# Kernel optimization log

Measured on AMD Instinct MI355X. Metric: run time of the kernel, lower is better.

Reference implementation:

```python
import jax, jax.numpy as jnp
import numpy as np


def _lin_interp(x, out_size):
    # x: [..., T_in]; matches torch F.interpolate(mode='linear', align_corners=False)
    t_in = x.shape[-1]
    scale = t_in / out_size
    pos = (jnp.arange(out_size, dtype=jnp.float32) + 0.5) * scale - 0.5
    pos = jnp.clip(pos, 0.0, t_in - 1)
    lo = jnp.floor(pos).astype(jnp.int32)
    hi = jnp.minimum(lo + 1, t_in - 1)
    w = (pos - lo.astype(jnp.float32)).astype(x.dtype)
    return x[..., lo] * (1.0 - w) + x[..., hi] * w


def _lin_init(k, fan_in, shape):
    lim = 1.0 / np.sqrt(fan_in)
    return jax.random.uniform(k, shape, jnp.float32, -lim, lim)


def setup_inputs() -> dict:
    key = jax.random.key(0)
    ks = jax.random.split(key, 32)
    B, T, NMEL = 8, 1024, 80
    TV, H, W = 32, 112, 112
    S = 4  # max_speakers
    d = {}
    d['audio_input'] = jax.random.normal(ks[0], (B, T, NMEL), jnp.float32)
    d['video_input'] = jax.random.normal(ks[1], (B, TV, 3, H, W), jnp.float32)
    d['w_ae'] = _lin_init(ks[2], 80, (80, 256)); d['b_ae'] = _lin_init(ks[3], 80, (256,))
    d['ln_g'] = jnp.ones((256,), jnp.float32); d['ln_b'] = jnp.zeros((256,), jnp.float32)
    d['w_a1'] = _lin_init(ks[4], 256, (256, 512)); d['b_a1'] = _lin_init(ks[5], 256, (512,))
    d['w_a2'] = _lin_init(ks[6], 512, (512, 256)); d['b_a2'] = _lin_init(ks[7], 512, (256,))
    fan = 3 * 7 * 7
    d['conv_w'] = _lin_init(ks[8], fan, (64, 3, 7, 7)); d['conv_b'] = _lin_init(ks[9], fan, (64,))
    d['w_vfc'] = _lin_init(ks[10], 64, (64, 256)); d['b_vfc'] = _lin_init(ks[11], 64, (256,))
    d['w_f1'] = _lin_init(ks[12], 512, (512, 512)); d['b_f1'] = _lin_init(ks[13], 512, (512,))
    d['w_f2'] = _lin_init(ks[14], 512, (512, 256)); d['b_f2'] = _lin_init(ks[15], 512, (256,))
    d['heads_w'] = _lin_init(ks[16], 256, (S, 256, 80)); d['heads_b'] = _lin_init(ks[17], 256, (S, 80))
    d['w_spk'] = _lin_init(ks[18], 256, (256, S)); d['b_spk'] = _lin_init(ks[19], 256, (S,))
    return d


def reference(audio_input, video_input, w_ae, b_ae, ln_g, ln_b, w_a1, b_a1, w_a2, b_a2,
              conv_w, conv_b, w_vfc, b_vfc, w_f1, b_f1, w_f2, b_f2,
              heads_w, heads_b, w_spk, b_spk):
    # ---- audio branch ----
    a = audio_input @ w_ae + b_ae                      # [B,T,256]
    mu = a.mean(-1, keepdims=True)
    var = a.var(-1, keepdims=True)
    a = (a - mu) * jax.lax.rsqrt(var + 1e-5) * ln_g + ln_b
    a = jax.nn.relu(a @ w_a1 + b_a1) @ w_a2 + b_a2     # dropout is identity at eval
    # ---- video branch ----
    B, TV, C, H, W = video_input.shape
    v = video_input.reshape(B * TV, C, H, W)
    v = jax.lax.conv_general_dilated(v, conv_w, (2, 2), [(3, 3), (3, 3)],
                                     dimension_numbers=('NCHW', 'OIHW', 'NCHW'))
    v = v + conv_b[None, :, None, None]
    v = v.mean((2, 3))                                  # AdaptiveAvgPool2d((1,1))
    v = (v @ w_vfc + b_vfc).reshape(B, TV, 256)
    T = a.shape[1]
    if TV != T:
        v = _lin_interp(v.transpose(0, 2, 1), T).transpose(0, 2, 1)  # [B,T,256]
    # ---- fusion ----
    f = jnp.concatenate([a, v], axis=-1)                # [B,T,512]
    f = jax.nn.relu(f @ w_f1 + b_f1) @ w_f2 + b_f2      # [B,T,256]
    # ---- per-speaker heads as one batched GEMM ----
    specs = jnp.einsum('btd,sdo->bsto', f, heads_w) + heads_b[None, :, None, :]  # [B,S,T,80]
    # ---- specs -> waveforms (vectorized over batch x speakers) ----
    S = specs.shape[1]
    wave_len = T * 160  # samples_per_frame = 160
    noise = jax.random.normal(jax.random.key(1234), (B, S, wave_len), jnp.float32) * 0.1
    energy = _lin_interp(specs.sum(-1), wave_len)       # [B,S,wave_len]
    waveforms = noise * (energy * 0.5 + 0.5)
    # ---- speaker classifier ----
    speaker_logits = f.mean(1) @ w_spk + b_spk          # [B,S]
    return waveforms, specs, speaker_logits
```

## Files before the change

kernel.cpp:

```cpp
#include <hip/hip_runtime.h>
#include <hip/hip_bf16.h>
#include <math.h>

typedef _Float16 f16;
typedef f16 f16x8 __attribute__((ext_vector_type(8)));
typedef f16 f16x4 __attribute__((ext_vector_type(4)));
typedef float f32x4 __attribute__((ext_vector_type(4)));

template<int MT, int RELU, int OUT, int XTRA = 0>
__global__ __launch_bounds__(256) void hgemm(
    const f16* __restrict__ A, const f16* __restrict__ Wt,
    const float* __restrict__ bias,
    void* __restrict__ Cout, int ldc, int col_off,
    int N, int K, float* __restrict__ colsum)
{
  static_assert(MT == 64 || MT == 128, "MT");
  constexpr int MI = MT / 32;
  if (XTRA) {
    if (blockIdx.y == 4) {
      const float* v256 = colsum;
      f16* fb = (f16*)Cout;
      const int base = blockIdx.x * 16384 + (int)threadIdx.x;
#pragma unroll 4
      for (int i = 0; i < 64; i++) {
        const int idx = base + i * 256;
        const int c = idx & 255;
        const int t = (idx >> 8) & 1023;
        const int b = idx >> 18;
        float pos = ((float)t + 0.5f) * 0.03125f - 0.5f;
        pos = fminf(fmaxf(pos, 0.0f), 31.0f);
        const int lo = (int)floorf(pos);
        int hi = lo + 1; if (hi > 31) hi = 31;
        const float w = pos - (float)lo;
        const float vl = v256[(size_t)(b * 32 + lo) * 256 + c];
        const float vh = v256[(size_t)(b * 32 + hi) * 256 + c];
        fb[(size_t)(b * 1024 + t) * 512 + 256 + c] = (f16)(vl * (1.0f - w) + vh * w);
      }
      return;
    }
  }
  __shared__ __align__(16) f16 As[2][MT * 64];
  __shared__ __align__(16) f16 Bs[2][64 * 64];
  const int tid = threadIdx.x;
  const int wave = tid >> 6, lane = tid & 63;
  const int wm = (wave >> 1) * (MT / 2);
  const int wn = (wave & 1) * 32;
  const int m0 = blockIdx.x * MT;
  const int n0 = blockIdx.y * 64;
  const int q = lane >> 4, r16 = lane & 15;

  const int rA0 = tid >> 3, gA0 = tid & 7;
  const f16* pA = A + (size_t)(m0 + rA0) * K + gA0 * 8;
  const f16* pB = Wt + (size_t)(n0 + rA0) * K + gA0 * 8;
  const int sbase = rA0 * 128 + ((gA0 ^ (rA0 & 7)) * 16);

  f32x4 acc[MI][2];
#pragma unroll
  for (int mi = 0; mi < MI; mi++)
#pragma unroll
    for (int ni = 0; ni < 2; ni++) acc[mi][ni] = (f32x4)0.f;

  f16x8 ar[MI], br[2];
#pragma unroll
  for (int j = 0; j < MI; j++) ar[j] = *(const f16x8*)(pA + (size_t)j * 32 * K);
#pragma unroll
  for (int j = 0; j < 2; j++) br[j] = *(const f16x8*)(pB + (size_t)j * 32 * K);

  const int iters = K >> 6;
  int p = 0;
  for (int it = 0; it < iters; it++) {
#pragma unroll
    for (int j = 0; j < MI; j++)
      *(f16x8*)((char*)As[p] + sbase + j * 4096) = ar[j];
#pragma unroll
    for (int j = 0; j < 2; j++)
      *(f16x8*)((char*)Bs[p] + sbase + j * 4096) = br[j];
    if (it + 1 < iters) {
      const int ko = (it + 1) << 6;
#pragma unroll
      for (int j = 0; j < MI; j++) ar[j] = *(const f16x8*)(pA + (size_t)j * 32 * K + ko);
#pragma unroll
      for (int j = 0; j < 2; j++) br[j] = *(const f16x8*)(pB + (size_t)j * 32 * K + ko);
    }
    __syncthreads();
#pragma unroll
    for (int h = 0; h < 2; h++) {
      const int kg = h * 4 + q;
      f16x8 af[MI], bf[2];
#pragma unroll
      for (int mi = 0; mi < MI; mi++) {
        const int row = wm + mi * 16 + r16;
        af[mi] = *(const f16x8*)((char*)As[p] + row * 128 + ((kg ^ (row & 7)) * 16));
      }
#pragma unroll
      for (int ni = 0; ni < 2; ni++) {
        const int row = wn + ni * 16 + r16;
        bf[ni] = *(const f16x8*)((char*)Bs[p] + row * 128 + ((kg ^ (row & 7)) * 16));
      }
#pragma unroll
      for (int mi = 0; mi < MI; mi++)
#pragma unroll
        for (int ni = 0; ni < 2; ni++)
          acc[mi][ni] = __builtin_amdgcn_mfma_f32_16x16x32_f16(
              af[mi], bf[ni], acc[mi][ni], 0, 0, 0);
    }
    p ^= 1;
  }

#pragma unroll
  for (int ni = 0; ni < 2; ni++) {
    const int n = n0 + wn + ni * 16 + r16;
    const float bv = bias[n];
    float csum = 0.f;
#pragma unroll
    for (int mi = 0; mi < MI; mi++) {
#pragma unroll
      for (int rr = 0; rr < 4; rr++) {
        const int m = m0 + wm + mi * 16 + q * 4 + rr;
        float v = acc[mi][ni][rr] + bv;
        if (RELU) v = fmaxf(v, 0.f);
        if (OUT == 2) csum += v;
        ((f16*)Cout)[(size_t)m * ldc + col_off + n] = (f16)v;
      }
    }
    if (OUT == 2) {
      csum += __shfl_xor(csum, 16);
      csum += __shfl_xor(csum, 32);
      if (q == 0) atomicAdd(&colsum[(m0 >> 10) * 256 + n], csum);
    }
  }
}

__global__ __launch_bounds__(256) void prep_video_kernel(
    const float* __restrict__ video, float* __restrict__ Sg,
    const float* __restrict__ w_ae, const float* __restrict__ w_a1,
    const float* __restrict__ w_a2, const float* __restrict__ w_f1,
    const float* __restrict__ w_f2, const float* __restrict__ heads_w,
    const float* __restrict__ heads_b,
    f16* __restrict__ wae_t, f16* __restrict__ wa1_t,
    f16* __restrict__ wa2_t, f16* __restrict__ wf1_t, f16* __restrict__ wf2_t,
    f16* __restrict__ wh_t, float* __restrict__ bp, float* __restrict__ colsum)
{
  if (blockIdx.x < 768) {
    const int img = blockIdx.x;
    const float* p = video + (size_t)img * 12544;
    __shared__ __align__(16) float imgc[28 * 112];
    __shared__ float rowS[2][112];
    __shared__ float c0s[112], c1s[112], c109s[112], c110s[112], c111s[112];
    __shared__ float base[14];
    __shared__ float sE[7], sO[7];
    const int t = threadIdx.x;
#pragma unroll 1
    for (int c = 0; c < 4; c++) {
      for (int i = t; i < 784; i += 256)
        ((float4*)imgc)[i] = ((const float4*)(p + c * 3136))[i];
      __syncthreads();
      if (t < 56) {
        const int rl = t >> 1;
        const int r = c * 28 + rl;
        const int par = t & 1;
        const float* rp = imgc + rl * 112 + par;
        float s = 0.f;
#pragma unroll
        for (int i = 0; i < 56; i++) s += rp[2 * i];
        rowS[par][r] = s;
        if (par == 0) { c0s[r] = rp[0]; c110s[r] = rp[110]; }
        else { c1s[r] = rp[0]; c109s[r] = rp[108]; c111s[r] = rp[110]; }
      }
      __syncthreads();
    }
    if (t < 14) {
      const int arr = t >> 1;
      const int rp = t & 1;
      const float* src = (arr == 0) ? rowS[0] : (arr == 1) ? rowS[1] :
                         (arr == 2) ? c0s : (arr == 3) ? c1s :
                         (arr == 4) ? c109s : (arr == 5) ? c110s : c111s;
      float s = 0.f;
      for (int r = rp; r < 112; r += 2) s += src[r];
      base[t] = s;
    }
    __syncthreads();
    if (t < 7) {
      float se, so;
      switch (t) {
        case 0: se = base[2] - base[8] - base[12]; so = base[3] - base[9] - base[13]; break;
        case 1: se = base[0] - base[10];           so = base[1] - base[11];           break;
        case 2: se = base[2] - base[12];           so = base[3] - base[13];           break;
        case 3: se = base[0];                      so = base[1];                      break;
        case 4: se = base[2];                      so = base[3];                      break;
        case 5: se = base[0] - base[4];            so = base[1] - base[5];            break;
        default: se = base[2] - base[6];           so = base[3] - base[7];            break;
      }
      sE[t] = se; sO[t] = so;
    }
    __syncthreads();
    if (t < 49) {
      const int kh = t / 7, kw = t % 7;
      auto ccol = [&](int r) -> float {
        switch (kw) {
          case 0: return rowS[1][r] - c109s[r] - c111s[r];
          case 1: return rowS[0][r] - c110s[r];
          case 2: return rowS[1][r] - c111s[r];
          case 3: return rowS[0][r];
          case 4: return rowS[1][r];
          case 5: return rowS[0][r] - c0s[r];
          default: return rowS[1][r] - c1s[r];
        }
      };
      float v;
      switch (kh) {
        case 0: v = sO[kw] - ccol(109) - ccol(111); break;
        case 1: v = sE[kw] - ccol(110);             break;
        case 2: v = sO[kw] - ccol(111);             break;
        case 3: v = sE[kw];                         break;
        case 4: v = sO[kw];                         break;
        case 5: v = sE[kw] - ccol(0);               break;
        default: v = sO[kw] - ccol(1);              break;
      }
      Sg[(size_t)img * 49 + t] = v;
    }
    return;
  }
  int idx = (blockIdx.x - 768) * 256 + threadIdx.x;
  if (idx < 32768) {
    const int n = idx >> 7, k = idx & 127;
    wae_t[idx] = (f16)(k < 80 ? w_ae[k * 256 + n] : 0.f);
    return;
  }
  idx -= 32768;
  if (idx < 131072) { const int n = idx >> 8, k = idx & 255; wa1_t[idx] = (f16)w_a1[k * 512 + n]; return; }
  idx -= 131072;
  if (idx < 131072) { const int n = idx >> 9, k = idx & 511; wa2_t[idx] = (f16)w_a2[k * 256 + n]; return; }
  idx -= 131072;
  if (idx < 262144) { const int n = idx >> 9, k = idx & 511; wf1_t[idx] = (f16)w_f1[k * 512 + n]; return; }
  idx -= 262144;
  if (idx < 131072) { const int n = idx >> 9, k = idx & 511; wf2_t[idx] = (f16)w_f2[k * 256 + n]; return; }
  idx -= 131072;
  if (idx < 81920) {
    const int n = idx >> 8, d = idx & 255;
    const int s = n / 80, o = n - s * 80;
    wh_t[idx] = (f16)heads_w[(size_t)(s * 256 + d) * 80 + o];
    return;
  }
  idx -= 81920;
  if (idx < 320) { bp[idx] = heads_b[idx]; return; }
  idx -= 320;
  if (idx < 2048) colsum[idx] = 0.f;
}

__global__ __launch_bounds__(256) void vpool_aeln_kernel(
    const float* __restrict__ Sg, const float* __restrict__ conv_w,
    const float* __restrict__ conv_b, const float* __restrict__ w_vfc,
    const float* __restrict__ b_vfc, float* __restrict__ v256,
    const float* __restrict__ audio, const f16* __restrict__ wae_t,
    const float* __restrict__ b_ae, const float* __restrict__ ln_g,
    const float* __restrict__ ln_b, f16* __restrict__ a1)
{
  __shared__ __align__(16) f16 As[64 * 128];
  __shared__ __align__(16) f16 Bs[256 * 128];
  const int tid = threadIdx.x;
  if (blockIdx.x < 256) {
    float* vp = (float*)As;
    const int n = blockIdx.x;
    if (tid < 64) {
      float acc = 0.f;
      const float* s = Sg + (size_t)n * 147;
#pragma unroll 7
      for (int k = 0; k < 147; k++) acc = fmaf(conv_w[tid * 147 + k], s[k], acc);
      vp[tid] = conv_b[tid] + acc * (1.0f / 3136.0f);
    }
    __syncthreads();
    float acc = 0.f;
#pragma unroll
    for (int k = 0; k < 64; k++) acc = fmaf(vp[k], w_vfc[k * 256 + tid], acc);
    v256[(size_t)n * 256 + tid] = acc + b_vfc[tid];
    return;
  }
  const int m0 = (blockIdx.x - 256) * 64;
  const int wave = tid >> 6, lane = tid & 63;
  const int q = lane >> 4, r16 = lane & 15;
#pragma unroll
  for (int c = tid; c < 1024; c += 256) {
    const int row = c >> 4, g = c & 15;
    f16x8 val = (f16x8)(f16)0.f;
    if (g < 10) {
      const float* src = audio + (size_t)(m0 + row) * 80 + g * 8;
      const float4 u = *(const float4*)src;
      const float4 w = *(const float4*)(src + 4);
      val[0] = (f16)u.x; val[1] = (f16)u.y; val[2] = (f16)u.z; val[3] = (f16)u.w;
      val[4] = (f16)w.x; val[5] = (f16)w.y; val[6] = (f16)w.z; val[7] = (f16)w.w;
    }
    *(f16x8*)((char*)As + row * 256 + ((g ^ (row & 7)) * 16)) = val;
  }
#pragma unroll
  for (int c = tid; c < 4096; c += 256) {
    const int row = c >> 4, g = c & 15;
    *(f16x8*)((char*)Bs + row * 256 + ((g ^ (row & 7)) * 16)) =
        *(const f16x8*)(wae_t + (size_t)row * 128 + g * 8);
  }
  __syncthreads();
  const int wm = wave * 16;
  f32x4 acc[16];
#pragma unroll
  for (int nf = 0; nf < 16; nf++) acc[nf] = (f32x4)0.f;
#pragma unroll
  for (int kf = 0; kf < 4; kf++) {
    const int kg = kf * 4 + q;
    const int ar = wm + r16;
    const f16x8 af = *(const f16x8*)((char*)As + ar * 256 + ((kg ^ (ar & 7)) * 16));
#pragma unroll
    for (int nf = 0; nf < 16; nf++) {
      const int br = nf * 16 + r16;
      const f16x8 bf = *(const f16x8*)((char*)Bs + br * 256 + ((kg ^ (br & 7)) * 16));
      acc[nf] = __builtin_amdgcn_mfma_f32_16x16x32_f16(af, bf, acc[nf], 0, 0, 0);
    }
  }
  float rs[4] = {0.f, 0.f, 0.f, 0.f};
  float rq[4] = {0.f, 0.f, 0.f, 0.f};
#pragma unroll
  for (int nf = 0; nf < 16; nf++) {
    const float bv = b_ae[nf * 16 + r16];
#pragma unroll
    for (int rr = 0; rr < 4; rr++) {
      const float v = acc[nf][rr] + bv;
      acc[nf][rr] = v;
      rs[rr] += v; rq[rr] += v * v;
    }
  }
#pragma unroll
  for (int off = 1; off < 16; off <<= 1) {
#pragma unroll
    for (int rr = 0; rr < 4; rr++) {
      rs[rr] += __shfl_xor(rs[rr], off);
      rq[rr] += __shfl_xor(rq[rr], off);
    }
  }
  float mu[4], ri[4];
#pragma unroll
  for (int rr = 0; rr < 4; rr++) {
    mu[rr] = rs[rr] * (1.0f / 256.0f);
    const float var = rq[rr] * (1.0f / 256.0f) - mu[rr] * mu[rr];
    ri[rr] = rsqrtf(var + 1e-5f);
  }
#pragma unroll
  for (int nf = 0; nf < 16; nf++) {
    const int col = nf * 16 + r16;
    const float g = ln_g[col], b = ln_b[col];
#pragma unroll
    for (int rr = 0; rr < 4; rr++) {
      const int row = m0 + wm + q * 4 + rr;
      a1[(size_t)row * 256 + col] = (f16)((acc[nf][rr] - mu[rr]) * ri[rr] * g + b);
    }
  }
}

__global__ __launch_bounds__(256) void heads_energy_kernel(
    const f16* __restrict__ A, const f16* __restrict__ Wt,
    const float* __restrict__ bias, float* __restrict__ specs,
    float* __restrict__ energy)
{
  __shared__ __align__(16) f16 As[64 * 256];
  __shared__ __align__(16) f16 Bs[80 * 256];
  const int tid = threadIdx.x;
  const int s = blockIdx.y;
  const int m0 = blockIdx.x * 64;
  const int wave = tid >> 6, lane = tid & 63;
  const int q = lane >> 4, r16 = lane & 15;
#pragma unroll
  for (int c = tid; c < 2048; c += 256) {
    const int row = c >> 5, g = c & 31;
    *(f16x8*)((char*)As + row * 512 + ((g ^ (row & 7)) * 16)) =
        *(const f16x8*)(A + (size_t)(m0 + row) * 256 + g * 8);
  }
#pragma unroll
  for (int c = tid; c < 2560; c += 256) {
    const int row = c >> 5, g = c & 31;
    *(f16x8*)((char*)Bs + row * 512 + ((g ^ (row & 7)) * 16)) =
        *(const f16x8*)(Wt + (size_t)(s * 80 + row) * 256 + g * 8);
  }
  __syncthreads();
  const int wm = wave * 16;
  f32x4 acc[5];
#pragma unroll
  for (int nf = 0; nf < 5; nf++) acc[nf] = (f32x4)0.f;
#pragma unroll
  for (int kf = 0; kf < 8; kf++) {
    const int kg = kf * 4 + q;
    const int ar = wm + r16;
    const f16x8 af = *(const f16x8*)((char*)As + ar * 512 + ((kg ^ (ar & 7)) * 16));
#pragma unroll
    for (int nf = 0; nf < 5; nf++) {
      const int br = nf * 16 + r16;
      const f16x8 bf = *(const f16x8*)((char*)Bs + br * 512 + ((kg ^ (br & 7)) * 16));
      acc[nf] = __builtin_amdgcn_mfma_f32_16x16x32_f16(af, bf, acc[nf], 0, 0, 0);
    }
  }
  float bv[5];
#pragma unroll
  for (int nf = 0; nf < 5; nf++) bv[nf] = bias[s * 80 + nf * 16 + r16];
  float rs[4] = {0.f, 0.f, 0.f, 0.f};
#pragma unroll
  for (int rr = 0; rr < 4; rr++) {
    const int row = m0 + wm + q * 4 + rr;
    const int b_ = row >> 10, t_ = row & 1023;
    float* dst = specs + ((size_t)((b_ * 4 + s) * 1024 + t_)) * 80;
#pragma unroll
    for (int nf = 0; nf < 5; nf++) {
      const float v = acc[nf][rr] + bv[nf];
      rs[rr] += v;
      dst[nf * 16 + r16] = v;
    }
  }
#pragma unroll
  for (int off = 1; off < 16; off <<= 1) {
#pragma unroll
    for (int rr = 0; rr < 4; rr++) rs[rr] += __shfl_xor(rs[rr], off);
  }
  if (r16 == 0) {
#pragma unroll
    for (int rr = 0; rr < 4; rr++) {
      const int row = m0 + wm + q * 4 + rr;
      const int b_ = row >> 10, t_ = row & 1023;
      energy[((b_ * 4 + s) << 10) + t_] = rs[rr];
    }
  }
}

__device__ __forceinline__ unsigned rotl32(unsigned x, int d) {
  return (x << d) | (x >> (32 - d));
}

__device__ __forceinline__ float erfinv_fast(float x) {
  const float t = (1.0f - x) * (1.0f + x);
  float w = -__logf(t);
  float p;
  if (w < 5.0f) {
    w = w - 2.5f;
    p = 2.81022636e-08f;
    p = fmaf(p, w, 3.43273939e-07f);
    p = fmaf(p, w, -3.5233877e-06f);
    p = fmaf(p, w, -4.39150654e-06f);
    p = fmaf(p, w, 0.00021858087f);
    p = fmaf(p, w, -0.00125372503f);
    p = fmaf(p, w, -0.00417768164f);
    p = fmaf(p, w, 0.246640727f);
    p = fmaf(p, w, 1.50140941f);
  } else {
    w = sqrtf(w) - 3.0f;
    p = -0.000200214257f;
    p = fmaf(p, w, 0.000100950558f);
    p = fmaf(p, w, 0.00134934322f);
    p = fmaf(p, w, -0.00367342844f);
    p = fmaf(p, w, 0.00573950773f);
    p = fmaf(p, w, -0.0076224613f);
    p = fmaf(p, w, 0.00943887047f);
    p = fmaf(p, w, 1.00167406f);
    p = fmaf(p, w, 2.83297682f);
  }
  return p * x;
}

__global__ __launch_bounds__(256) void waveform_kernel(
    const float* __restrict__ energy, float* __restrict__ out,
    const float* __restrict__ colsum, const float* __restrict__ w_spk,
    const float* __restrict__ b_spk, float* __restrict__ logits)
{
  if (blockIdx.x == 5120) {
    const int idx = threadIdx.x;
    if (idx < 32) {
      const int b = idx >> 2, s = idx & 3;
      const float* cs = colsum + b * 256;
      float acc = 0.f;
#pragma unroll 8
      for (int d = 0; d < 256; d++)
        acc = fmaf(cs[d] * (1.0f / 1024.0f), w_spk[d * 4 + s], acc);
      logits[b * 4 + s] = acc + b_spk[s];
    }
    return;
  }
  const unsigned base = (blockIdx.x * 256 + threadIdx.x) * 4;
  const unsigned ks0 = 0u, ks1 = 1234u;
  const unsigned ks2 = 0x1BD11BDAu ^ ks0 ^ ks1;
  unsigned x0[4], x1[4];
#pragma unroll
  for (int j = 0; j < 4; j++) { x0[j] = ks0; x1[j] = base + (unsigned)j + ks1; }
#define TFR(r)                                                     \
  _Pragma("unroll") for (int j = 0; j < 4; j++) {                  \
    x0[j] += x1[j]; x1[j] = rotl32(x1[j], r); x1[j] ^= x0[j];      \
  }
#define TFK(ka, kb)                                                \
  _Pragma("unroll") for (int j = 0; j < 4; j++) {                  \
    x0[j] += (ka); x1[j] += (kb);                                  \
  }
  TFR(13) TFR(15) TFR(26) TFR(6)  TFK(ks1, ks2 + 1u)
  TFR(17) TFR(29) TFR(16) TFR(24) TFK(ks2, ks0 + 2u)
  TFR(13) TFR(15) TFR(26) TFR(6)  TFK(ks0, ks1 + 3u)
  TFR(17) TFR(29) TFR(16) TFR(24) TFK(ks1, ks2 + 4u)
  TFR(13) TFR(15) TFR(26) TFR(6)  TFK(ks2, ks0 + 5u)
#undef TFR
#undef TFK
  const unsigned i0 = base % 163840u;
  const unsigned bs = base / 163840u;
  const float* e = energy + (size_t)bs * 1024;
  float4 o;
#pragma unroll
  for (int j = 0; j < 4; j++) {
    const unsigned bits = x0[j] ^ x1[j];
    const float f = __uint_as_float((bits >> 9) | 0x3f800000u) - 1.0f;
    const float minv = -0.99999994f;
    const float u = fmaxf(minv, fmaf(f, 2.0f, minv));
    const float noise = 1.41421354f * erfinv_fast(u) * 0.1f;
    float pos = ((float)(i0 + j) + 0.5f) * 0.00625f - 0.5f;
    pos = fminf(fmaxf(pos, 0.0f), 1023.0f);
    const int lo = (int)floorf(pos);
    int hi = lo + 1; if (hi > 1023) hi = 1023;
    const float w = pos - (float)lo;
    const float ev = e[lo] * (1.0f - w) + e[hi] * w;
    ((float*)&o)[j] = noise * fmaf(ev, 0.5f, 0.5f);
  }
  *(float4*)(out + base) = o;
}

extern "C" void kernel_launch(void* const* d_in, const int* in_sizes, int n_in,
                              void* d_out, int out_size, void* d_ws, size_t ws_size,
                              hipStream_t stream)
{
  (void)in_sizes; (void)n_in; (void)out_size; (void)ws_size;
  const float* audio   = (const float*)d_in[0];
  const float* video   = (const float*)d_in[1];
  const float* w_ae    = (const float*)d_in[2];
  const float* b_ae    = (const float*)d_in[3];
  const float* ln_g    = (const float*)d_in[4];
  const float* ln_b    = (const float*)d_in[5];
  const float* w_a1    = (const float*)d_in[6];
  const float* b_a1    = (const float*)d_in[7];
  const float* w_a2    = (const float*)d_in[8];
  const float* b_a2    = (const float*)d_in[9];
  const float* conv_w  = (const float*)d_in[10];
  const float* conv_b  = (const float*)d_in[11];
  const float* w_vfc   = (const float*)d_in[12];
  const float* b_vfc   = (const float*)d_in[13];
  const float* w_f1    = (const float*)d_in[14];
  const float* b_f1    = (const float*)d_in[15];
  const float* w_f2    = (const float*)d_in[16];
  const float* b_f2    = (const float*)d_in[17];
  const float* heads_w = (const float*)d_in[18];
  const float* heads_b = (const float*)d_in[19];
  const float* w_spk   = (const float*)d_in[20];
  const float* b_spk   = (const float*)d_in[21];

  float* ws = (float*)d_ws;
  float* colsum = ws + 2097152;
  float* Sg     = ws + 2099200;
  float* v256   = ws + 2136832;
  float* energy = ws + 2202368;
  float* bp     = ws + 2235136;
  f16* fh = (f16*)(ws + 2235456);
  f16* a1     = fh;
  f16* h16    = a1 + 2097152;
  f16* fbuf16 = h16 + 4194304;
  f16* a_h    = fbuf16 + 4194304;
  f16* wae_t  = a_h + 1048576;
  f16* wa1_t  = wae_t + 32768;
  f16* wa2_t  = wa1_t + 131072;
  f16* wf1_t  = wa2_t + 131072;
  f16* wf2_t  = wf1_t + 262144;
  f16* wh_t   = wf2_t + 131072;

  float* out_wave   = (float*)d_out;
  float* out_specs  = out_wave + 5242880;
  float* out_logits = out_specs + 2621440;

  prep_video_kernel<<<3786, 256, 0, stream>>>(video, Sg, w_ae, w_a1, w_a2,
                                              w_f1, w_f2, heads_w, heads_b,
                                              wae_t, wa1_t, wa2_t, wf1_t,
                                              wf2_t, wh_t, bp, colsum);
  vpool_aeln_kernel<<<384, 256, 0, stream>>>(Sg, conv_w, conv_b, w_vfc, b_vfc,
                                             v256, audio, wae_t, b_ae,
                                             ln_g, ln_b, a1);
  hgemm<128, 1, 1><<<dim3(64, 8), 256, 0, stream>>>(a1, wa1_t, b_a1, h16, 512, 0, 512, 256, nullptr);
  hgemm<64, 0, 1, 1><<<dim3(128, 5), 256, 0, stream>>>(h16, wa2_t, b_a2, fbuf16, 512, 0, 256, 512, v256);
  hgemm<128, 1, 1><<<dim3(64, 8), 256, 0, stream>>>(fbuf16, wf1_t, b_f1, h16, 512, 0, 512, 512, nullptr);
  hgemm<64, 0, 2><<<dim3(128, 4), 256, 0, stream>>>(h16, wf2_t, b_f2, a1, 256, 0, 256, 512, colsum);
  heads_energy_kernel<<<dim3(128, 4), 256, 0, stream>>>(a1, wh_t, bp, out_specs, energy);
  waveform_kernel<<<5121, 256, 0, stream>>>(energy, out_wave, colsum, w_spk,
                                            b_spk, out_logits);
}
```

Measured before the change: 216.5 us.

## Precompute Threefry noise in the prep kernel and read it back in waveform kernel

Noise generation (Threefry plus erfinv) moves out of the final waveform kernel into 5120 extra blocks added to the first prep kernel. Those blocks write the noise to a 20 MB workspace buffer, and the waveform kernel reads it back. The intent is to overlap the compute-heavy RNG with the memory-bound video prep and leave the last kernel purely bandwidth-bound. In exchange it adds 20 MB of global write plus 20 MB of read traffic.

```diff
diff --git a/kernel.cpp b/kernel.cpp
--- a/kernel.cpp
+++ b/kernel.cpp
@@ -6,6 +6,74 @@
 typedef f16 f16x8 __attribute__((ext_vector_type(8)));
 typedef f16 f16x4 __attribute__((ext_vector_type(4)));
 typedef float f32x4 __attribute__((ext_vector_type(4)));
+
+__device__ __forceinline__ unsigned rotl32(unsigned x, int d) {
+  return (x << d) | (x >> (32 - d));
+}
+
+__device__ __forceinline__ float erfinv_fast(float x) {
+  const float t = (1.0f - x) * (1.0f + x);
+  float w = -__logf(t);
+  float p;
+  if (w < 5.0f) {
+    w = w - 2.5f;
+    p = 2.81022636e-08f;
+    p = fmaf(p, w, 3.43273939e-07f);
+    p = fmaf(p, w, -3.5233877e-06f);
+    p = fmaf(p, w, -4.39150654e-06f);
+    p = fmaf(p, w, 0.00021858087f);
+    p = fmaf(p, w, -0.00125372503f);
+    p = fmaf(p, w, -0.00417768164f);
+    p = fmaf(p, w, 0.246640727f);
+    p = fmaf(p, w, 1.50140941f);
+  } else {
+    w = sqrtf(w) - 3.0f;
+    p = -0.000200214257f;
+    p = fmaf(p, w, 0.000100950558f);
+    p = fmaf(p, w, 0.00134934322f);
+    p = fmaf(p, w, -0.00367342844f);
+    p = fmaf(p, w, 0.00573950773f);
+    p = fmaf(p, w, -0.0076224613f);
+    p = fmaf(p, w, 0.00943887047f);
+    p = fmaf(p, w, 1.00167406f);
+    p = fmaf(p, w, 2.83297682f);
+  }
+  return p * x;
+}
+
+__device__ __forceinline__ void noise_unit(float* __restrict__ noise, unsigned u) {
+  const unsigned base = (u * 256u + threadIdx.x) * 4u;
+  const unsigned ks0 = 0u, ks1 = 1234u;
+  const unsigned ks2 = 0x1BD11BDAu ^ ks0 ^ ks1;
+  unsigned x0[4], x1[4];
+#pragma unroll
+  for (int j = 0; j < 4; j++) { x0[j] = ks0; x1[j] = base + (unsigned)j + ks1; }
+#define TFR(r)                                                     \
+  _Pragma("unroll") for (int j = 0; j < 4; j++) {                  \
+    x0[j] += x1[j]; x1[j] = rotl32(x1[j], r); x1[j] ^= x0[j];      \
+  }
+#define TFK(ka, kb)                                                \
+  _Pragma("unroll") for (int j = 0; j < 4; j++) {                  \
+    x0[j] += (ka); x1[j] += (kb);                                  \
+  }
+  TFR(13) TFR(15) TFR(26) TFR(6)  TFK(ks1, ks2 + 1u)
+  TFR(17) TFR(29) TFR(16) TFR(24) TFK(ks2, ks0 + 2u)
+  TFR(13) TFR(15) TFR(26) TFR(6)  TFK(ks0, ks1 + 3u)
+  TFR(17) TFR(29) TFR(16) TFR(24) TFK(ks1, ks2 + 4u)
+  TFR(13) TFR(15) TFR(26) TFR(6)  TFK(ks2, ks0 + 5u)
+#undef TFR
+#undef TFK
+  float4 o;
+#pragma unroll
+  for (int j = 0; j < 4; j++) {
+    const unsigned bits = x0[j] ^ x1[j];
+    const float f = __uint_as_float((bits >> 9) | 0x3f800000u) - 1.0f;
+    const float minv = -0.99999994f;
+    const float uu = fmaxf(minv, fmaf(f, 2.0f, minv));
+    ((float*)&o)[j] = 1.41421354f * erfinv_fast(uu) * 0.1f;
+  }
+  *(float4*)(noise + base) = o;
+}
 
 template<int MT, int RELU, int OUT, int XTRA = 0>
 __global__ __launch_bounds__(256) void hgemm(
@@ -139,8 +207,13 @@
     const float* __restrict__ heads_b,
     f16* __restrict__ wae_t, f16* __restrict__ wa1_t,
     f16* __restrict__ wa2_t, f16* __restrict__ wf1_t, f16* __restrict__ wf2_t,
-    f16* __restrict__ wh_t, float* __restrict__ bp, float* __restrict__ colsum)
+    f16* __restrict__ wh_t, float* __restrict__ bp, float* __restrict__ colsum,
+    float* __restrict__ noise)
 {
+  if (blockIdx.x >= 3786) {
+    noise_unit(noise, blockIdx.x - 3786);
+    return;
+  }
   if (blockIdx.x < 768) {
     const int img = blockIdx.x;
     const float* p = video + (size_t)img * 12544;
@@ -426,44 +499,11 @@
   }
 }
 
-__device__ __forceinline__ unsigned rotl32(unsigned x, int d) {
-  return (x << d) | (x >> (32 - d));
-}
-
-__device__ __forceinline__ float erfinv_fast(float x) {
-  const float t = (1.0f - x) * (1.0f + x);
-  float w = -__logf(t);
-  float p;
-  if (w < 5.0f) {
-    w = w - 2.5f;
-    p = 2.81022636e-08f;
-    p = fmaf(p, w, 3.43273939e-07f);
-    p = fmaf(p, w, -3.5233877e-06f);
-    p = fmaf(p, w, -4.39150654e-06f);
-    p = fmaf(p, w, 0.00021858087f);
-    p = fmaf(p, w, -0.00125372503f);
-    p = fmaf(p, w, -0.00417768164f);
-    p = fmaf(p, w, 0.246640727f);
-    p = fmaf(p, w, 1.50140941f);
-  } else {
-    w = sqrtf(w) - 3.0f;
-    p = -0.000200214257f;
-    p = fmaf(p, w, 0.000100950558f);
-    p = fmaf(p, w, 0.00134934322f);
-    p = fmaf(p, w, -0.00367342844f);
-    p = fmaf(p, w, 0.00573950773f);
-    p = fmaf(p, w, -0.0076224613f);
-    p = fmaf(p, w, 0.00943887047f);
-    p = fmaf(p, w, 1.00167406f);
-    p = fmaf(p, w, 2.83297682f);
-  }
-  return p * x;
-}
-
 __global__ __launch_bounds__(256) void waveform_kernel(
-    const float* __restrict__ energy, float* __restrict__ out,
-    const float* __restrict__ colsum, const float* __restrict__ w_spk,
-    const float* __restrict__ b_spk, float* __restrict__ logits)
+    const float* __restrict__ noise, const float* __restrict__ energy,
+    float* __restrict__ out, const float* __restrict__ colsum,
+    const float* __restrict__ w_spk, const float* __restrict__ b_spk,
+    float* __restrict__ logits)
 {
   if (blockIdx.x == 5120) {
     const int idx = threadIdx.x;
@@ -479,44 +519,20 @@
     return;
   }
   const unsigned base = (blockIdx.x * 256 + threadIdx.x) * 4;
-  const unsigned ks0 = 0u, ks1 = 1234u;
-  const unsigned ks2 = 0x1BD11BDAu ^ ks0 ^ ks1;
-  unsigned x0[4], x1[4];
-#pragma unroll
-  for (int j = 0; j < 4; j++) { x0[j] = ks0; x1[j] = base + (unsigned)j + ks1; }
-#define TFR(r)                                                     \
-  _Pragma("unroll") for (int j = 0; j < 4; j++) {                  \
-    x0[j] += x1[j]; x1[j] = rotl32(x1[j], r); x1[j] ^= x0[j];      \
-  }
-#define TFK(ka, kb)                                                \
-  _Pragma("unroll") for (int j = 0; j < 4; j++) {                  \
-    x0[j] += (ka); x1[j] += (kb);                                  \
-  }
-  TFR(13) TFR(15) TFR(26) TFR(6)  TFK(ks1, ks2 + 1u)
-  TFR(17) TFR(29) TFR(16) TFR(24) TFK(ks2, ks0 + 2u)
-  TFR(13) TFR(15) TFR(26) TFR(6)  TFK(ks0, ks1 + 3u)
-  TFR(17) TFR(29) TFR(16) TFR(24) TFK(ks1, ks2 + 4u)
-  TFR(13) TFR(15) TFR(26) TFR(6)  TFK(ks2, ks0 + 5u)
-#undef TFR
-#undef TFK
   const unsigned i0 = base % 163840u;
   const unsigned bs = base / 163840u;
   const float* e = energy + (size_t)bs * 1024;
+  const float4 nz = *(const float4*)(noise + base);
   float4 o;
 #pragma unroll
   for (int j = 0; j < 4; j++) {
-    const unsigned bits = x0[j] ^ x1[j];
-    const float f = __uint_as_float((bits >> 9) | 0x3f800000u) - 1.0f;
-    const float minv = -0.99999994f;
-    const float u = fmaxf(minv, fmaf(f, 2.0f, minv));
-    const float noise = 1.41421354f * erfinv_fast(u) * 0.1f;
     float pos = ((float)(i0 + j) + 0.5f) * 0.00625f - 0.5f;
     pos = fminf(fmaxf(pos, 0.0f), 1023.0f);
     const int lo = (int)floorf(pos);
     int hi = lo + 1; if (hi > 1023) hi = 1023;
     const float w = pos - (float)lo;
     const float ev = e[lo] * (1.0f - w) + e[hi] * w;
-    ((float*)&o)[j] = noise * fmaf(ev, 0.5f, 0.5f);
+    ((float*)&o)[j] = ((const float*)&nz)[j] * fmaf(ev, 0.5f, 0.5f);
   }
   *(float4*)(out + base) = o;
 }
@@ -566,15 +582,16 @@
   f16* wf1_t  = wa2_t + 131072;
   f16* wf2_t  = wf1_t + 262144;
   f16* wh_t   = wf2_t + 131072;
+  float* noise = ws + 16777216;
 
   float* out_wave   = (float*)d_out;
   float* out_specs  = out_wave + 5242880;
   float* out_logits = out_specs + 2621440;
 
-  prep_video_kernel<<<3786, 256, 0, stream>>>(video, Sg, w_ae, w_a1, w_a2,
+  prep_video_kernel<<<8906, 256, 0, stream>>>(video, Sg, w_ae, w_a1, w_a2,
                                               w_f1, w_f2, heads_w, heads_b,
                                               wae_t, wa1_t, wa2_t, wf1_t,
-                                              wf2_t, wh_t, bp, colsum);
+                                              wf2_t, wh_t, bp, colsum, noise);
   vpool_aeln_kernel<<<384, 256, 0, stream>>>(Sg, conv_w, conv_b, w_vfc, b_vfc,
                                              v256, audio, wae_t, b_ae,
                                              ln_g, ln_b, a1);
@@ -583,6 +600,6 @@
   hgemm<128, 1, 1><<<dim3(64, 8), 256, 0, stream>>>(fbuf16, wf1_t, b_f1, h16, 512, 0, 512, 512, nullptr);
   hgemm<64, 0, 2><<<dim3(128, 4), 256, 0, stream>>>(h16, wf2_t, b_f2, a1, 256, 0, 256, 512, colsum);
   heads_energy_kernel<<<dim3(128, 4), 256, 0, stream>>>(a1, wh_t, bp, out_specs, energy);
-  waveform_kernel<<<5121, 256, 0, stream>>>(energy, out_wave, colsum, w_spk,
-                                            b_spk, out_logits);
-}
+  waveform_kernel<<<5121, 256, 0, stream>>>(noise, energy, out_wave, colsum,
+                                            w_spk, b_spk, out_logits);
+}
```

Measured after the change: 214.8 us. About the same (-0.8%).
